# Performance work log

Measured on AMD Instinct MI355X. Metric: run time of the kernel, lower is better.

Reference implementation:

```python
import jax, jax.numpy as jnp
import numpy as np

NUM_USERS = 30000
NUM_ITEMS = 30000
N = NUM_USERS + NUM_ITEMS          # total graph nodes (users + items)
E = 800000                          # number of edges
EMBED_K = 64
INTENTS = 4
D = EMBED_K // INTENTS              # per-intent channel chunk
N_LAYERS = 1
ROUTING_ITERS = 2


def setup_inputs() -> dict:
    key = jax.random.key(0)
    k1, k2, k3, k4 = jax.random.split(key, 4)
    Gu = jax.random.normal(k1, (NUM_USERS, EMBED_K), jnp.float32) * 0.1
    Gi = jax.random.normal(k2, (NUM_ITEMS, EMBED_K), jnp.float32) * 0.1
    # head list: guarantee every node appears at least once as a head so that
    # D = 1/sqrt(row_degree) is finite (real CF graphs have no isolated rows)
    edge_h = jnp.concatenate([jnp.arange(N, dtype=jnp.int64),
                              jax.random.randint(k3, (E - N,), 0, N, dtype=jnp.int64)])
    edge_t = jax.random.randint(k4, (E,), 0, N, dtype=jnp.int64)
    return {"Gu": Gu, "Gi": Gi, "edge_h": edge_h, "edge_t": edge_t}


def _l2norm(x, eps=1e-12):
    # matches torch.nn.functional.normalize(dim=-1)
    return x / jnp.sqrt(jnp.maximum(jnp.sum(x * x, axis=-1, keepdims=True), eps))


def reference(Gu, Gi, edge_h, edge_t):
    ego = jnp.concatenate([Gu, Gi], axis=0)            # [N, K]
    all_emb = [ego]
    # routing attention logits per intent per edge (initialized to ones)
    A_values = jnp.ones((INTENTS, E), dtype=Gu.dtype)
    for _ in range(N_LAYERS):
        # split embed dim into INTENTS contiguous chunks -> [I, N, D]
        X = ego.reshape(N, INTENTS, D).transpose(1, 0, 2)
        Z = X
        for _t in range(ROUTING_ITERS):
            # softmax over intents per edge (pick=False path; p_train is always False)
            scores = jax.nn.softmax(A_values, axis=0)                    # [I, E]
            # per-intent row degrees (sparse.sum over dim=1 indexes rows = heads)
            deg = jnp.zeros((INTENTS, N), scores.dtype).at[:, edge_h].add(scores)
            d_col = 1.0 / jnp.sqrt(deg)                                  # [I, N]
            # D_col @ X, A @ (.), D_col @ (.)  -- note original applies D_col twice (as written)
            Y = d_col[..., None] * X                                     # [I, N, D]
            msg = scores[..., None] * Y[:, edge_t, :]                    # [I, E, D]
            Z = jnp.zeros((INTENTS, N, D), X.dtype).at[:, edge_h, :].add(msg)
            Z = d_col[..., None] * Z                                     # [I, N, D]
            # attention update: normalize(head) . tanh(normalize(tail))
            head = _l2norm(Z[:, edge_h, :])                              # [I, E, D]
            tail = _l2norm(X[:, edge_t, :])                              # [I, E, D]
            A_values = A_values + jnp.sum(head * jnp.tanh(tail), axis=-1)
        # concat intent chunks back along channel dim
        ego = Z.transpose(1, 0, 2).reshape(N, EMBED_K)
        all_emb.append(ego)
    out = jnp.mean(jnp.stack(all_emb, axis=1), axis=1)   # [N, K]
    return out[:NUM_USERS], out[NUM_USERS:]
```

## Files before the change

### kernel.cpp

```cpp
#include <hip/hip_runtime.h>
#include <hip/hip_fp16.h>


#define NUSERS 30000
#define NN     60000
#define EE     800000
#define SCAN_B ((NN + 255) / 256)
#define EV_B   ((EE / 4 + 255) / 256)
#define NW1_B  ((NN + 1 + 3) / 4)
#define N8_B   ((NN + 7) / 8)

__device__ __forceinline__ float getX(const float* __restrict__ Gu,
                                      const float* __restrict__ Gi,
                                      int n, int c) {
    return (n < NUSERS) ? Gu[n * 64 + c] : Gi[(n - NUSERS) * 64 + c];
}

__device__ __forceinline__ int clampN(int n) {
    return ((unsigned)n < (unsigned)NN) ? n : 0;
}

__device__ __forceinline__ __half2 bch2(float f) {
    return __builtin_bit_cast(__half2, f);
}


__global__ void edge_count(const int* __restrict__ eh, int* __restrict__ deg0,
                           int* __restrict__ rank) {
    int e4 = (blockIdx.x * blockDim.x + threadIdx.x) * 4;
    if (e4 >= EE) return;
    int4 h = *(const int4*)(eh + e4);
    int4 r;
    r.x = atomicAdd(&deg0[clampN(h.x)], 1);
    r.y = atomicAdd(&deg0[clampN(h.y)], 1);
    r.z = atomicAdd(&deg0[clampN(h.z)], 1);
    r.w = atomicAdd(&deg0[clampN(h.w)], 1);
    *(int4*)(rank + e4) = r;
}

__global__ void scan_local(const int* __restrict__ deg0, int* __restrict__ offsets,
                           int* __restrict__ bsum) {
    int gid = blockIdx.x * 256 + threadIdx.x;
    int lane = threadIdx.x & 63, w = threadIdx.x >> 6;
    int vdeg = (gid < NN) ? deg0[gid] : 0;
    int x = vdeg;
    #pragma unroll
    for (int d = 1; d < 64; d <<= 1) {
        int y = __shfl_up(x, d, 64);
        if (lane >= d) x += y;
    }
    __shared__ int wsum[4];
    if (lane == 63) wsum[w] = x;
    __syncthreads();
    int wpre = 0;
    #pragma unroll
    for (int j = 0; j < 4; ++j) wpre += (j < w) ? wsum[j] : 0;
    int incl = x + wpre;
    if (gid < NN) offsets[gid] = incl - vdeg;
    if (threadIdx.x == 255) bsum[blockIdx.x] = incl;
}

__global__ void scan_add2(int* __restrict__ offsets, const int* __restrict__ bsum) {
    int tid = threadIdx.x, lane = tid & 63, w = tid >> 6;
    int vv = (tid < SCAN_B) ? bsum[tid] : 0;
    int x = vv;
    #pragma unroll
    for (int d = 1; d < 64; d <<= 1) {
        int y = __shfl_up(x, d, 64);
        if (lane >= d) x += y;
    }
    __shared__ int wsum[4];
    __shared__ int bpre;
    if (lane == 63) wsum[w] = x;
    __syncthreads();
    int wpre = 0;
    #pragma unroll
    for (int j = 0; j < 4; ++j) wpre += (j < w) ? wsum[j] : 0;
    if (tid == blockIdx.x) bpre = x + wpre - vv;
    __syncthreads();
    int gid = blockIdx.x * 256 + tid;
    if (gid < NN) offsets[gid] += bpre;
    if (gid == 0) offsets[NN] = EE;
}

__global__ void scatter_prep(const int* __restrict__ eh, const int* __restrict__ et,
                             const int* __restrict__ rank,
                             const int* __restrict__ offsets,
                             int* __restrict__ csr_tail,
                             const float* __restrict__ Gu, const float* __restrict__ Gi,
                             const int* __restrict__ deg0,
                             __half* __restrict__ Ytab, __half* __restrict__ Ttab) {
    if (blockIdx.x < EV_B) {
        int e4 = (blockIdx.x * 256 + threadIdx.x) * 4;
        if (e4 >= EE) return;
        int4 h = *(const int4*)(eh + e4);
        int4 t = *(const int4*)(et + e4);
        int4 r = *(const int4*)(rank + e4);
        int s0 = offsets[clampN(h.x)] + r.x;
        if ((unsigned)s0 < EE) csr_tail[s0] = clampN(t.x);
        int s1 = offsets[clampN(h.y)] + r.y;
        if ((unsigned)s1 < EE) csr_tail[s1] = clampN(t.y);
        int s2 = offsets[clampN(h.z)] + r.z;
        if ((unsigned)s2 < EE) csr_tail[s2] = clampN(t.z);
        int s3 = offsets[clampN(h.w)] + r.w;
        if ((unsigned)s3 < EE) csr_tail[s3] = clampN(t.w);
    } else {
        int n = (blockIdx.x - EV_B) * 4 + (threadIdx.x >> 6);
        if (n > NN) return;
        int lane = threadIdx.x & 63;
        float x = (n < NN) ? getX(Gu, Gi, n, lane) : 0.f;
        float sx = x * x;
        #pragma unroll
        for (int m = 1; m < 16; m <<= 1) sx += __shfl_xor(sx, m, 64);
        float invx = rsqrtf(fmaxf(sx, 1e-12f));
        float d0 = rsqrtf(fmaxf(0.25f * (float)((n < NN) ? deg0[n] : 1), 1e-30f));
        size_t a = (size_t)n * 64 + lane;
        Ytab[a] = __float2half(d0 * x);
        Ttab[a] = __float2half(tanhf(x * invx));
    }
}

__global__ void zacc(const int* __restrict__ offsets, const int* __restrict__ csr_tail,
                     const __half* __restrict__ Ytab, __half* __restrict__ ZN,
                     int* __restrict__ csr_head) {
    int tid = threadIdx.x;
    int n = blockIdx.x * 8 + (tid >> 5);
    if (n >= NN) return;
    int cc = tid & 31;
    int s0 = offsets[n], s1 = offsets[n + 1];
    for (int k = s0 + cc; k < s1; k += 32) csr_head[k] = n;
    float accx = 0.f, accy = 0.f;
    for (int base = s0; base < s1; base += 4) {
        #pragma unroll
        for (int u = 0; u < 4; ++u) {
            int kk = base + u;
            bool act = kk < s1;
            int kc = act ? kk : s0;
            int t = act ? csr_tail[kc] : NN;
            __half2 y = *(const __half2*)(Ytab + (size_t)t * 64 + cc * 2);
            float2 yf = __half22float2(y);
            accx += yf.x; accy += yf.y;
        }
    }
    float ss = accx * accx + accy * accy;
    ss += __shfl_xor(ss, 1, 64);
    ss += __shfl_xor(ss, 2, 64);
    ss += __shfl_xor(ss, 4, 64);
    float inv = rsqrtf(fmaxf(ss, 1e-12f));
    *(__half2*)(ZN + (size_t)n * 64 + cc * 2) =
        __floats2half2_rn(accx * inv, accy * inv);
}

__global__ void attdot_sm(const int* __restrict__ csr_head, const int* __restrict__ csr_tail,
                          const __half* __restrict__ ZN, const __half* __restrict__ Ttab,
                          __half* __restrict__ s4) {
    int k = blockIdx.x * 256 + threadIdx.x;
    if (k >= EE) return;
    int h = csr_head[k], t = csr_tail[k];
    const float4* zp = (const float4*)(ZN + (size_t)h * 64);
    const float4* tp = (const float4*)(Ttab + (size_t)t * 64);
    float dot[4];
    #pragma unroll
    for (int i = 0; i < 4; ++i) {
        float4 za = zp[2 * i], zb = zp[2 * i + 1];
        float4 ta = tp[2 * i], tb = tp[2 * i + 1];
        __half2 acc = __floats2half2_rn(0.f, 0.f);
        acc = __hfma2(bch2(za.x), bch2(ta.x), acc);
        acc = __hfma2(bch2(za.y), bch2(ta.y), acc);
        acc = __hfma2(bch2(za.z), bch2(ta.z), acc);
        acc = __hfma2(bch2(za.w), bch2(ta.w), acc);
        acc = __hfma2(bch2(zb.x), bch2(tb.x), acc);
        acc = __hfma2(bch2(zb.y), bch2(tb.y), acc);
        acc = __hfma2(bch2(zb.z), bch2(tb.z), acc);
        acc = __hfma2(bch2(zb.w), bch2(tb.w), acc);
        float2 f = __half22float2(acc);
        dot[i] = f.x + f.y;
    }
    float mx = fmaxf(fmaxf(dot[0], dot[1]), fmaxf(dot[2], dot[3]));
    float e0 = __expf(dot[0] - mx), e1 = __expf(dot[1] - mx);
    float e2 = __expf(dot[2] - mx), e3 = __expf(dot[3] - mx);
    float inv = 1.f / (e0 + e1 + e2 + e3);
    __half2 q01 = __floats2half2_rn(e0 * inv, e1 * inv);
    __half2 q23 = __floats2half2_rn(e2 * inv, e3 * inv);
    int2 st;
    st.x = __builtin_bit_cast(int, q01);
    st.y = __builtin_bit_cast(int, q23);
    *(int2*)(s4 + (size_t)k * 4) = st;
}

__global__ void deg_y1(const int* __restrict__ offsets, const __half* __restrict__ s4,
                       float* __restrict__ dcol1,
                       const float* __restrict__ Gu, const float* __restrict__ Gi,
                       __half* __restrict__ Y1i) {
    int n = blockIdx.x * 4 + (threadIdx.x >> 6);
    if (n >= NN) return;
    int lane = threadIdx.x & 63;
    int s0 = offsets[n], s1 = offsets[n + 1];
    float sum0 = 0.f, sum1 = 0.f, sum2 = 0.f, sum3 = 0.f;
    for (int k = s0 + lane; k < s1; k += 64) {
        int2 raw = *(const int2*)(s4 + (size_t)k * 4);
        float2 fa = __half22float2(__builtin_bit_cast(__half2, raw.x));
        float2 fb = __half22float2(__builtin_bit_cast(__half2, raw.y));
        sum0 += fa.x; sum1 += fa.y; sum2 += fb.x; sum3 += fb.y;
    }
    #pragma unroll
    for (int m = 1; m < 64; m <<= 1) {
        sum0 += __shfl_xor(sum0, m, 64);
        sum1 += __shfl_xor(sum1, m, 64);
        sum2 += __shfl_xor(sum2, m, 64);
        sum3 += __shfl_xor(sum3, m, 64);
    }
    int i = lane >> 4;
    float dsel = (i == 0) ? sum0 : (i == 1) ? sum1 : (i == 2) ? sum2 : sum3;
    float d = rsqrtf(fmaxf(dsel, 1e-30f));
    if (lane < 4) {
        float ds = (lane == 0) ? sum0 : (lane == 1) ? sum1 : (lane == 2) ? sum2 : sum3;
        dcol1[n * 4 + lane] = rsqrtf(fmaxf(ds, 1e-30f));
    }
    float x = getX(Gu, Gi, n, lane);
    Y1i[(size_t)n * 64 + lane] = __float2half(d * x);
}

__global__ void outk(const int* __restrict__ offsets, const int* __restrict__ csr_tail,
                     const __half* __restrict__ Y1i, const __half* __restrict__ s4,
                     const float* __restrict__ dcol1,
                     const float* __restrict__ Gu, const float* __restrict__ Gi,
                     float* __restrict__ out) {
    int tid = threadIdx.x;
    int n = blockIdx.x * 8 + (tid >> 5);
    if (n >= NN) return;
    int cc = tid & 31;
    int s0 = offsets[n], s1 = offsets[n + 1];
    float accx = 0.f, accy = 0.f;
    for (int base = s0; base < s1; base += 4) {
        #pragma unroll
        for (int u = 0; u < 4; ++u) {
            int kk = base + u;
            bool act = kk < s1;
            int kc = act ? kk : s0;
            int t = csr_tail[kc];
            int2 raw = *(const int2*)(s4 + (size_t)kc * 4);
            int word = (cc & 16) ? raw.y : raw.x;
            unsigned short us = (unsigned short)(word >> ((cc & 8) ? 16 : 0));
            float s = act ? __half2float(__builtin_bit_cast(__half, us)) : 0.f;
            __half2 y = *(const __half2*)(Y1i + (size_t)t * 64 + cc * 2);
            float2 yf = __half22float2(y);
            accx = fmaf(s, yf.x, accx);
            accy = fmaf(s, yf.y, accy);
        }
    }
    float d = dcol1[n * 4 + (cc >> 3)];
    int ch = cc * 2;
    const float* xr = (n < NUSERS) ? (Gu + (size_t)n * 64 + ch)
                                   : (Gi + (size_t)(n - NUSERS) * 64 + ch);
    float2 x2 = *(const float2*)xr;
    float2 o;
    o.x = 0.5f * (x2.x + d * accx);
    o.y = 0.5f * (x2.y + d * accy);
    *(float2*)(out + (size_t)n * 64 + ch) = o;
}


extern "C" void kernel_launch(void* const* d_in, const int* in_sizes, int n_in,
                              void* d_out, int out_size, void* d_ws, size_t ws_size,
                              hipStream_t stream) {
    const float* Gu = (const float*)d_in[0];
    const float* Gi = (const float*)d_in[1];
    const int* eh = (const int*)d_in[2];
    const int* et = (const int*)d_in[3];
    float* out = (float*)d_out;

    char* p = (char*)d_ws;
    __half* s4       = (__half*)p;     p += (size_t)EE * 4 * 2;
    int*    csr_tail = (int*)p;        p += (size_t)EE * 4;
    int*    csr_head = (int*)p;        p += (size_t)EE * 4;
    int*    rank     = (int*)p;        p += (size_t)EE * 4;
    int*    offsets  = (int*)p;        p += ((size_t)(NN + 1) * 4 + 15) / 16 * 16;
    int*    deg0     = (int*)p;        p += (size_t)NN * 4;
    int*    bsum     = (int*)p;        p += ((size_t)SCAN_B * 4 + 15) / 16 * 16;
    float*  dcol1    = (float*)p;      p += (size_t)NN * 4 * 4;
    __half* Ytab     = (__half*)p;     p += (size_t)(NN + 1) * 64 * 2;
    __half* Ttab     = (__half*)p;     p += (size_t)(NN + 1) * 64 * 2;
    __half* ZN       = (__half*)p;
    __half* Y1i      = Ytab;

    const int nw_blocks = (NN + 3) / 4;

    hipMemsetAsync(deg0, 0, NN * sizeof(int), stream);
    edge_count<<<EV_B, 256, 0, stream>>>(eh, deg0, rank);
    scan_local<<<SCAN_B, 256, 0, stream>>>(deg0, offsets, bsum);
    scan_add2<<<SCAN_B, 256, 0, stream>>>(offsets, bsum);

    scatter_prep<<<EV_B + NW1_B, 256, 0, stream>>>(eh, et, rank, offsets, csr_tail,
                                                   Gu, Gi, deg0, Ytab, Ttab);

    zacc<<<N8_B, 256, 0, stream>>>(offsets, csr_tail, Ytab, ZN, csr_head);
    attdot_sm<<<(EE + 255) / 256, 256, 0, stream>>>(csr_head, csr_tail, ZN, Ttab, s4);

    deg_y1<<<nw_blocks, 256, 0, stream>>>(offsets, s4, dcol1, Gu, Gi, Y1i);

    outk<<<N8_B, 256, 0, stream>>>(offsets, csr_tail, Y1i, s4, dcol1, Gu, Gi, out);
}
```

Before: 252.7 us.

## Fuse head aggregation, attention softmax and degree pass into one block kernel

Merges zacc, attdot_sm and deg_y1 into a single kernel where each block handles eight consecutive head nodes. The normalized head vectors stay in shared memory instead of going to a global ZN buffer, and per-node score sums are built with shared-memory atomics. This removes the csr_head array and two kernel launches, and drops the global head-vector gathers and the s4 re-read. The cost is load imbalance from per-block edge ranges, shared atomics contention, and a per-edge linear search to find the local head. Y1i now gets its own buffer instead of aliasing Ytab.

```diff
diff --git a/kernel.cpp b/kernel.cpp
--- a/kernel.cpp
+++ b/kernel.cpp
@@ -8,7 +8,7 @@
 #define SCAN_B ((NN + 255) / 256)
 #define EV_B   ((EE / 4 + 255) / 256)
 #define NW1_B  ((NN + 1 + 3) / 4)
-#define N8_B   ((NN + 7) / 8)
+#define N8_B   (NN / 8)
 
 __device__ __forceinline__ float getX(const float* __restrict__ Gu,
                                       const float* __restrict__ Gi,
@@ -120,105 +120,100 @@
     }
 }
 
-__global__ void zacc(const int* __restrict__ offsets, const int* __restrict__ csr_tail,
-                     const __half* __restrict__ Ytab, __half* __restrict__ ZN,
-                     int* __restrict__ csr_head) {
+__global__ void zat(const int* __restrict__ offsets, const int* __restrict__ csr_tail,
+                    const __half* __restrict__ Ytab, const __half* __restrict__ Ttab,
+                    __half* __restrict__ s4, float* __restrict__ dcol1,
+                    const float* __restrict__ Gu, const float* __restrict__ Gi,
+                    __half* __restrict__ Y1i) {
+    __shared__ __half zn[8][72];
+    __shared__ float ssum[8][4];
+    __shared__ int soff[9];
     int tid = threadIdx.x;
-    int n = blockIdx.x * 8 + (tid >> 5);
-    if (n >= NN) return;
-    int cc = tid & 31;
-    int s0 = offsets[n], s1 = offsets[n + 1];
-    for (int k = s0 + cc; k < s1; k += 32) csr_head[k] = n;
-    float accx = 0.f, accy = 0.f;
-    for (int base = s0; base < s1; base += 4) {
-        #pragma unroll
-        for (int u = 0; u < 4; ++u) {
-            int kk = base + u;
-            bool act = kk < s1;
-            int kc = act ? kk : s0;
-            int t = act ? csr_tail[kc] : NN;
-            __half2 y = *(const __half2*)(Ytab + (size_t)t * 64 + cc * 2);
-            float2 yf = __half22float2(y);
-            accx += yf.x; accy += yf.y;
+    int n0 = blockIdx.x * 8;
+    if (tid < 9) soff[tid] = offsets[n0 + tid];
+    if (tid >= 32 && tid < 64) ssum[(tid - 32) >> 2][tid & 3] = 0.f;
+    __syncthreads();
+
+    {
+        int g = tid >> 5, cc = tid & 31;
+        int s0 = soff[g], s1 = soff[g + 1];
+        float accx = 0.f, accy = 0.f;
+        for (int base = s0; base < s1; base += 4) {
+            #pragma unroll
+            for (int u = 0; u < 4; ++u) {
+                int kk = base + u;
+                bool act = kk < s1;
+                int kc = act ? kk : s0;
+                int t = act ? csr_tail[kc] : NN;
+                __half2 y = *(const __half2*)(Ytab + (size_t)t * 64 + cc * 2);
+                float2 yf = __half22float2(y);
+                accx += yf.x; accy += yf.y;
+            }
         }
-    }
-    float ss = accx * accx + accy * accy;
-    ss += __shfl_xor(ss, 1, 64);
-    ss += __shfl_xor(ss, 2, 64);
-    ss += __shfl_xor(ss, 4, 64);
-    float inv = rsqrtf(fmaxf(ss, 1e-12f));
-    *(__half2*)(ZN + (size_t)n * 64 + cc * 2) =
-        __floats2half2_rn(accx * inv, accy * inv);
-}
-
-__global__ void attdot_sm(const int* __restrict__ csr_head, const int* __restrict__ csr_tail,
-                          const __half* __restrict__ ZN, const __half* __restrict__ Ttab,
-                          __half* __restrict__ s4) {
-    int k = blockIdx.x * 256 + threadIdx.x;
-    if (k >= EE) return;
-    int h = csr_head[k], t = csr_tail[k];
-    const float4* zp = (const float4*)(ZN + (size_t)h * 64);
-    const float4* tp = (const float4*)(Ttab + (size_t)t * 64);
-    float dot[4];
-    #pragma unroll
-    for (int i = 0; i < 4; ++i) {
-        float4 za = zp[2 * i], zb = zp[2 * i + 1];
-        float4 ta = tp[2 * i], tb = tp[2 * i + 1];
-        __half2 acc = __floats2half2_rn(0.f, 0.f);
-        acc = __hfma2(bch2(za.x), bch2(ta.x), acc);
-        acc = __hfma2(bch2(za.y), bch2(ta.y), acc);
-        acc = __hfma2(bch2(za.z), bch2(ta.z), acc);
-        acc = __hfma2(bch2(za.w), bch2(ta.w), acc);
-        acc = __hfma2(bch2(zb.x), bch2(tb.x), acc);
-        acc = __hfma2(bch2(zb.y), bch2(tb.y), acc);
-        acc = __hfma2(bch2(zb.z), bch2(tb.z), acc);
-        acc = __hfma2(bch2(zb.w), bch2(tb.w), acc);
-        float2 f = __half22float2(acc);
-        dot[i] = f.x + f.y;
-    }
-    float mx = fmaxf(fmaxf(dot[0], dot[1]), fmaxf(dot[2], dot[3]));
-    float e0 = __expf(dot[0] - mx), e1 = __expf(dot[1] - mx);
-    float e2 = __expf(dot[2] - mx), e3 = __expf(dot[3] - mx);
-    float inv = 1.f / (e0 + e1 + e2 + e3);
-    __half2 q01 = __floats2half2_rn(e0 * inv, e1 * inv);
-    __half2 q23 = __floats2half2_rn(e2 * inv, e3 * inv);
-    int2 st;
-    st.x = __builtin_bit_cast(int, q01);
-    st.y = __builtin_bit_cast(int, q23);
-    *(int2*)(s4 + (size_t)k * 4) = st;
-}
-
-__global__ void deg_y1(const int* __restrict__ offsets, const __half* __restrict__ s4,
-                       float* __restrict__ dcol1,
-                       const float* __restrict__ Gu, const float* __restrict__ Gi,
-                       __half* __restrict__ Y1i) {
-    int n = blockIdx.x * 4 + (threadIdx.x >> 6);
-    if (n >= NN) return;
-    int lane = threadIdx.x & 63;
-    int s0 = offsets[n], s1 = offsets[n + 1];
-    float sum0 = 0.f, sum1 = 0.f, sum2 = 0.f, sum3 = 0.f;
-    for (int k = s0 + lane; k < s1; k += 64) {
-        int2 raw = *(const int2*)(s4 + (size_t)k * 4);
-        float2 fa = __half22float2(__builtin_bit_cast(__half2, raw.x));
-        float2 fb = __half22float2(__builtin_bit_cast(__half2, raw.y));
-        sum0 += fa.x; sum1 += fa.y; sum2 += fb.x; sum3 += fb.y;
-    }
-    #pragma unroll
-    for (int m = 1; m < 64; m <<= 1) {
-        sum0 += __shfl_xor(sum0, m, 64);
-        sum1 += __shfl_xor(sum1, m, 64);
-        sum2 += __shfl_xor(sum2, m, 64);
-        sum3 += __shfl_xor(sum3, m, 64);
-    }
-    int i = lane >> 4;
-    float dsel = (i == 0) ? sum0 : (i == 1) ? sum1 : (i == 2) ? sum2 : sum3;
-    float d = rsqrtf(fmaxf(dsel, 1e-30f));
-    if (lane < 4) {
-        float ds = (lane == 0) ? sum0 : (lane == 1) ? sum1 : (lane == 2) ? sum2 : sum3;
-        dcol1[n * 4 + lane] = rsqrtf(fmaxf(ds, 1e-30f));
-    }
-    float x = getX(Gu, Gi, n, lane);
-    Y1i[(size_t)n * 64 + lane] = __float2half(d * x);
+        float ss = accx * accx + accy * accy;
+        ss += __shfl_xor(ss, 1, 64);
+        ss += __shfl_xor(ss, 2, 64);
+        ss += __shfl_xor(ss, 4, 64);
+        float inv = rsqrtf(fmaxf(ss, 1e-12f));
+        *(__half2*)&zn[g][cc * 2] = __floats2half2_rn(accx * inv, accy * inv);
+    }
+    __syncthreads();
+
+    int e0 = soff[0], e1 = soff[8];
+    for (int k = e0 + tid; k < e1; k += 256) {
+        int hl = 0;
+        #pragma unroll
+        for (int j = 1; j < 8; ++j) hl += (k >= soff[j]) ? 1 : 0;
+        int t = csr_tail[k];
+        const float4* tp = (const float4*)(Ttab + (size_t)t * 64);
+        float dot[4];
+        #pragma unroll
+        for (int i = 0; i < 4; ++i) {
+            float4 za = *(const float4*)&zn[hl][i * 16];
+            float4 zb = *(const float4*)&zn[hl][i * 16 + 8];
+            float4 ta = tp[2 * i], tb = tp[2 * i + 1];
+            __half2 acc = __floats2half2_rn(0.f, 0.f);
+            acc = __hfma2(bch2(za.x), bch2(ta.x), acc);
+            acc = __hfma2(bch2(za.y), bch2(ta.y), acc);
+            acc = __hfma2(bch2(za.z), bch2(ta.z), acc);
+            acc = __hfma2(bch2(za.w), bch2(ta.w), acc);
+            acc = __hfma2(bch2(zb.x), bch2(tb.x), acc);
+            acc = __hfma2(bch2(zb.y), bch2(tb.y), acc);
+            acc = __hfma2(bch2(zb.z), bch2(tb.z), acc);
+            acc = __hfma2(bch2(zb.w), bch2(tb.w), acc);
+            float2 f = __half22float2(acc);
+            dot[i] = f.x + f.y;
+        }
+        float mx = fmaxf(fmaxf(dot[0], dot[1]), fmaxf(dot[2], dot[3]));
+        float q0 = __expf(dot[0] - mx), q1 = __expf(dot[1] - mx);
+        float q2 = __expf(dot[2] - mx), q3 = __expf(dot[3] - mx);
+        float inv = 1.f / (q0 + q1 + q2 + q3);
+        q0 *= inv; q1 *= inv; q2 *= inv; q3 *= inv;
+        __half2 o01 = __floats2half2_rn(q0, q1);
+        __half2 o23 = __floats2half2_rn(q2, q3);
+        int2 st;
+        st.x = __builtin_bit_cast(int, o01);
+        st.y = __builtin_bit_cast(int, o23);
+        *(int2*)(s4 + (size_t)k * 4) = st;
+        atomicAdd(&ssum[hl][0], q0);
+        atomicAdd(&ssum[hl][1], q1);
+        atomicAdd(&ssum[hl][2], q2);
+        atomicAdd(&ssum[hl][3], q3);
+    }
+    __syncthreads();
+
+    if (tid < 32) {
+        int nn = n0 + (tid >> 2);
+        dcol1[nn * 4 + (tid & 3)] = rsqrtf(fmaxf(ssum[tid >> 2][tid & 3], 1e-30f));
+    }
+    #pragma unroll
+    for (int v = tid; v < 512; v += 256) {
+        int nn = n0 + (v >> 6);
+        int ch = v & 63;
+        float d = rsqrtf(fmaxf(ssum[v >> 6][ch >> 4], 1e-30f));
+        float x = getX(Gu, Gi, nn, ch);
+        Y1i[(size_t)nn * 64 + ch] = __float2half(d * x);
+    }
 }
 
 __global__ void outk(const int* __restrict__ offsets, const int* __restrict__ csr_tail,
@@ -273,7 +268,6 @@
     char* p = (char*)d_ws;
     __half* s4       = (__half*)p;     p += (size_t)EE * 4 * 2;
     int*    csr_tail = (int*)p;        p += (size_t)EE * 4;
-    int*    csr_head = (int*)p;        p += (size_t)EE * 4;
     int*    rank     = (int*)p;        p += (size_t)EE * 4;
     int*    offsets  = (int*)p;        p += ((size_t)(NN + 1) * 4 + 15) / 16 * 16;
     int*    deg0     = (int*)p;        p += (size_t)NN * 4;
@@ -281,10 +275,7 @@
     float*  dcol1    = (float*)p;      p += (size_t)NN * 4 * 4;
     __half* Ytab     = (__half*)p;     p += (size_t)(NN + 1) * 64 * 2;
     __half* Ttab     = (__half*)p;     p += (size_t)(NN + 1) * 64 * 2;
-    __half* ZN       = (__half*)p;
-    __half* Y1i      = Ytab;
-
-    const int nw_blocks = (NN + 3) / 4;
+    __half* Y1i      = (__half*)p;
 
     hipMemsetAsync(deg0, 0, NN * sizeof(int), stream);
     edge_count<<<EV_B, 256, 0, stream>>>(eh, deg0, rank);
@@ -294,10 +285,8 @@
     scatter_prep<<<EV_B + NW1_B, 256, 0, stream>>>(eh, et, rank, offsets, csr_tail,
                                                    Gu, Gi, deg0, Ytab, Ttab);
 
-    zacc<<<N8_B, 256, 0, stream>>>(offsets, csr_tail, Ytab, ZN, csr_head);
-    attdot_sm<<<(EE + 255) / 256, 256, 0, stream>>>(csr_head, csr_tail, ZN, Ttab, s4);
-
-    deg_y1<<<nw_blocks, 256, 0, stream>>>(offsets, s4, dcol1, Gu, Gi, Y1i);
+    zat<<<N8_B, 256, 0, stream>>>(offsets, csr_tail, Ytab, Ttab, s4, dcol1,
+                                  Gu, Gi, Y1i);
 
     outk<<<N8_B, 256, 0, stream>>>(offsets, csr_tail, Y1i, s4, dcol1, Gu, Gi, out);
 }
```

Result: faster. 237.2 us (-6.2%).
